# Kernel optimization log

Hardware: AMD Instinct MI355X
Metric: run time of the kernel (lower is better)

The kernel has to match this reference:

```python
import jax, jax.numpy as jnp
import numpy as np

B, T, C, H, W = 16, 8, 16, 64, 64
HID = 32          # round(sqrt(num_audio_input_ch * num_latent_ch)) = sqrt(16*64)
LAT = 64          # num_latent_ch
K = 3             # kernel_size


def conv(x, w, b):
    # x: [B,Cin,H,W], w: [Cout,Cin,K,K] (OIHW), SAME padding == padding (1,1) for 3x3
    y = jax.lax.conv_general_dilated(x, w, (1, 1), 'SAME',
                                     dimension_numbers=('NCHW', 'OIHW', 'NCHW'))
    return y + b[None, :, None, None]


def lstm_scan(x_seq, w, b, hid):
    # x_seq: [T,B,Cin,H,W] -> hidden sequence [T,B,hid,H,W]
    Bn, Hh, Ww = x_seq.shape[1], x_seq.shape[3], x_seq.shape[4]
    h0 = jnp.zeros((Bn, hid, Hh, Ww), x_seq.dtype)

    def step(carry, x_t):
        h, c = carry
        z = conv(jnp.concatenate([x_t, h], axis=1), w, b)     # [B,4*hid,H,W]
        i, f, o, g = jnp.split(z, 4, axis=1)                   # gate order i,f,o,g
        c2 = jax.nn.sigmoid(f) * c + jax.nn.sigmoid(i) * jnp.tanh(g)
        h2 = jax.nn.sigmoid(o) * jnp.tanh(c2)
        return (h2, c2), h2

    _, hs = jax.lax.scan(step, (h0, h0), x_seq)
    return hs


def bidir_layer(x_seq, wf, bf, wb, bb, hid):
    hf = lstm_scan(x_seq, wf, bf, hid)
    hb = jnp.flip(lstm_scan(jnp.flip(x_seq, 0), wb, bb, hid), 0)
    return jnp.concatenate([hf, hb], axis=2)                   # [T,B,2*hid,H,W]


def setup_inputs() -> dict:
    key = jax.random.key(0)
    ks = jax.random.split(key, 16)
    s = 0.05
    pe_dim = C * H * W
    inp = {
        'x_audio': jax.random.normal(ks[0], (B, T, C, H, W), jnp.float32),
        'midi_notes': jax.random.uniform(ks[1], (B, T, 2), jnp.float32, 0.0, 127.0),
        # note encoder: Linear(2,4) -> ReLU -> Linear(4, C*H*W) -> Tanh
        'enc_w1': jax.random.normal(ks[2], (2, 4), jnp.float32) * s,
        'enc_b1': jnp.zeros((4,), jnp.float32),
        'enc_w2': jax.random.normal(ks[3], (4, pe_dim), jnp.float32) * s,
        'enc_b2': jnp.zeros((pe_dim,), jnp.float32),
        # layer 0 (input C=16), fwd + bwd cells
        'w0f': jax.random.normal(ks[4], (4 * HID, C + HID, K, K), jnp.float32) * s,
        'b0f': jnp.zeros((4 * HID,), jnp.float32),
        'w0b': jax.random.normal(ks[5], (4 * HID, C + HID, K, K), jnp.float32) * s,
        'b0b': jnp.zeros((4 * HID,), jnp.float32),
        # layer 1 (input 2*HID=64)
        'w1f': jax.random.normal(ks[6], (4 * HID, 2 * HID + HID, K, K), jnp.float32) * s,
        'b1f': jnp.zeros((4 * HID,), jnp.float32),
        'w1b': jax.random.normal(ks[7], (4 * HID, 2 * HID + HID, K, K), jnp.float32) * s,
        'b1b': jnp.zeros((4 * HID,), jnp.float32),
        # final conv: 2*HID -> LAT
        'fc_w': jax.random.normal(ks[8], (LAT, 2 * HID, K, K), jnp.float32) * s,
        'fc_b': jnp.zeros((LAT,), jnp.float32),
    }
    return inp


def reference(x_audio, midi_notes, enc_w1, enc_b1, enc_w2, enc_b2,
              w0f, b0f, w0b, b0b, w1f, b1f, w1b, b1b, fc_w, fc_b):
    # positional encoding from MIDI notes, vectorized over all timesteps
    notes = -0.5 + midi_notes / 64.0                              # [B,T,2]
    pe = jnp.tanh(jax.nn.relu(notes @ enc_w1 + enc_b1) @ enc_w2 + enc_b2)  # [B,T,C*H*W]
    x = x_audio + pe.reshape(x_audio.shape)
    xs = jnp.transpose(x, (1, 0, 2, 3, 4))                        # [T,B,C,H,W]
    h = bidir_layer(xs, w0f, b0f, w0b, b0b, HID)                  # [T,B,64,H,W]
    h = bidir_layer(h, w1f, b1f, w1b, b1b, HID)                   # [T,B,64,H,W]
    return conv(h[-1], fc_w, fc_b)                                # [B,LAT,H,W]
```

## Files before the change

kernel.cpp:

```cpp
#include <hip/hip_runtime.h>

typedef _Float16 f16;
typedef _Float16 f16x8 __attribute__((ext_vector_type(8)));
typedef float f32x16 __attribute__((ext_vector_type(16)));

namespace {

constexpr int B_ = 16, T_ = 8, HW = 4096;

__device__ __forceinline__ float sigm(float x)  { return 1.f / (1.f + __expf(-x)); }
__device__ __forceinline__ float ftanh(float x) { return 1.f - 2.f / (1.f + __expf(2.f * x)); }

__device__ __forceinline__ f32x16 zero16() {
  f32x16 v;
#pragma unroll
  for (int i = 0; i < 16; ++i) v[i] = 0.f;
  return v;
}

__device__ __forceinline__ f16x8 zero8h() {
  f16x8 v;
#pragma unroll
  for (int i = 0; i < 8; ++i) v[i] = (f16)0.f;
  return v;
}

struct WSet { const float* src; f16* dst; int KC, NCO, CIN; };

__global__ void warr_kernel(WSet s0, WSet s1, WSet s2, WSet s3, WSet s4) {
  WSet s = s0;
  switch (blockIdx.y) { case 1: s = s1; break; case 2: s = s2; break;
                        case 3: s = s3; break; case 4: s = s4; break; default: break; }
  int n = 9 * s.KC * s.NCO * 16;
  int i = blockIdx.x * 256 + threadIdx.x;
  if (i >= n) return;
  int kk = i & 15;
  int t = i >> 4;
  int co = t % s.NCO;
  int dkc = t / s.NCO;
  int kc = dkc % s.KC, dydx = dkc / s.KC;
  int ci = kc * 16 + kk;
  float v = (ci < s.CIN) ? s.src[(co * s.CIN + ci) * 9 + dydx] : 0.f;
  s.dst[i] = (f16)v;
}

__global__ void pe_kernel(const float* __restrict__ xa, const float* __restrict__ midi,
                          const float* __restrict__ w1, const float* __restrict__ b1,
                          const float* __restrict__ w2, const float* __restrict__ b2,
                          f16* __restrict__ xs) {
  int gid = blockIdx.x * 256 + threadIdx.x;
  int half = gid & 1;
  int gpx = gid >> 1;
  int bt = gpx >> 12, gp = gpx & 4095;
  float n0 = -0.5f + midi[bt * 2 + 0] * (1.f / 64.f);
  float n1 = -0.5f + midi[bt * 2 + 1] * (1.f / 64.f);
  float hk[4];
#pragma unroll
  for (int k = 0; k < 4; ++k)
    hk[k] = fmaxf(fmaf(n0, w1[k], fmaf(n1, w1[4 + k], b1[k])), 0.f);
  f16x8 ov;
#pragma unroll
  for (int j = 0; j < 8; ++j) {
    int c = half * 8 + j;
    long p = (long)c * HW + gp;
    float z = b2[p];
#pragma unroll
    for (int k = 0; k < 4; ++k) z = fmaf(hk[k], w2[(long)k * 65536 + p], z);
    ov[j] = (f16)(xa[(long)bt * 65536 + p] + ftanh(z));
  }
  *reinterpret_cast<f16x8*>(xs + (long)gpx * 16 + half * 8) = ov;
}

struct ConvDir {
  const f16* x;  long xbs;
  const f16* h;  long hbs;
  const f16* w;
  const float* bias;
  const f16* cin;
  f16* cout;
  float* fout;
  f16* hout; long hobs;
};

template<int CIN1, int CIN2, int CINPAD, int KCF, int KC, int HST, int HOST,
         bool GATES, int NCO>
__global__ __launch_bounds__(256, 2)
void conv_mfma(ConvDir p0, ConvDir p1)
{
  constexpr int MFRAG = 2;
  constexpr int NF = NCO / 64;
  constexpr int NPH = 9 * KC;
  constexpr int ACT_BYTES = 180 * CINPAD * 2;
  constexpr int ZB_BYTES  = GATES ? 128 * 128 * 2 : 0;
  constexpr int SMEM = ACT_BYTES > ZB_BYTES ? ACT_BYTES : ZB_BYTES;
  __shared__ __align__(16) char smem[SMEM];
  f16* act = (f16*)smem;
  f16* zls = (f16*)smem;

  const ConvDir P = blockIdx.y ? p1 : p0;
  const int b = blockIdx.z;
  const int tileY = blockIdx.x >> 2, tileX = blockIdx.x & 3;
  const int gy0 = tileY * 8, gx0 = tileX * 16;
  const int tid = threadIdx.x;

  const int lane = tid & 63, wv = tid >> 6;
  const int mg = wv & 1, ng = wv >> 1;
  const int rl = lane & 31;
  const int khalf = (lane >> 5) * 8;
  const int laneA = ((rl >> 4) * 18 + (rl & 15)) * CINPAD + khalf;
  const int laneB = rl * 16 + khalf;
  const f16* __restrict__ wng = P.w + laneB + (long)ng * NF * 32 * 16;
  const f16* __restrict__ arow = act + laneA;

  constexpr int UPX = CIN1 / 8, UPH = CIN2 / 8, UPP = UPX + UPH;
  constexpr int NU  = 180 * UPP;
  constexpr int PER = (NU + 255) / 256;
  const bool have_h = (P.h != nullptr);
  f16x8 sreg[PER];
#pragma unroll
  for (int p = 0; p < PER; ++p) {
    sreg[p] = zero8h();
    int i = tid + p * 256;
    if (i < NU) {
      int px = i / UPP, u = i - px * UPP;
      int py = px / 18, pxx = px - py * 18;
      int gy = gy0 + py - 1, gx = gx0 + pxx - 1;
      if ((unsigned)gy < 64u && (unsigned)gx < 64u && (u < UPX || have_h)) {
        long gp = (long)gy * 64 + gx;
        const f16* src = (u < UPX) ? (P.x + b * P.xbs + gp * CIN1 + u * 8)
                                   : (P.h + b * P.hbs + gp * HST + (u - UPX) * 8);
        sreg[p] = *reinterpret_cast<const f16x8*>(src);
      }
    }
  }

  f16x8 bfr[3][NF];
  f16x8 afr[2][MFRAG];

  auto LBF = [&](int ph) {
    const int slot = ph % 3;
    const int dydx = ph / KC, kc = ph % KC;
#pragma unroll
    for (int nf = 0; nf < NF; ++nf)
      bfr[slot][nf] = *reinterpret_cast<const f16x8*>(
          wng + ((long)(dydx * KCF + kc) * NCO + nf * 32) * 16);
  };
  auto LAF = [&](int ph) {
    const int slot = ph & 1;
    const int dydx = ph / KC, kc = ph % KC;
    const int dy = dydx / 3, dx = dydx % 3;
#pragma unroll
    for (int m = 0; m < MFRAG; ++m)
      afr[slot][m] = *reinterpret_cast<const f16x8*>(
          arow + dx * CINPAD + (((mg * MFRAG + m) * 2 + dy) * 18) * CINPAD + kc * 16);
  };

  LBF(0);
  if (NPH > 1) LBF(1);

#pragma unroll
  for (int p = 0; p < PER; ++p) {
    int i = tid + p * 256;
    if (i < NU) {
      int px = i / UPP, u = i - px * UPP;
      *reinterpret_cast<f16x8*>(act + px * CINPAD + u * 8) = sreg[p];
    }
  }
  __syncthreads();

  if (NPH > 2) LBF(2);

  f32x16 acc[MFRAG][NF];
#pragma unroll
  for (int m = 0; m < MFRAG; ++m)
#pragma unroll
    for (int nf = 0; nf < NF; ++nf) acc[m][nf] = zero16();

  LAF(0);
#pragma unroll
  for (int ph = 0; ph < NPH; ++ph) {
    if (ph + 1 < NPH) LAF(ph + 1);
#pragma unroll
    for (int m = 0; m < MFRAG; ++m)
#pragma unroll
      for (int nf = 0; nf < NF; ++nf)
        acc[m][nf] = __builtin_amdgcn_mfma_f32_32x32x16_f16(
            afr[ph & 1][m], bfr[ph % 3][nf], acc[m][nf], 0, 0, 0);
    if (ph + 3 < NPH) LBF(ph + 3);
  }

  __syncthreads();

  if constexpr (GATES) {
#pragma unroll
    for (int m = 0; m < MFRAG; ++m) {
#pragma unroll
      for (int nf = 0; nf < NF; ++nf) {
        const int col = (ng * NF + nf) * 32 + rl;
        const float bs = P.bias[col];
#pragma unroll
        for (int r = 0; r < 16; ++r) {
          int row = (r & 3) + 8 * (r >> 2) + 4 * (lane >> 5);
          int px = (mg * MFRAG + m) * 32 + row;
          zls[px * 128 + col] = (f16)(acc[m][nf][r] + bs);
        }
      }
    }
    __syncthreads();
#pragma unroll
    for (int it = 0; it < 2; ++it) {
      const int idx = tid + it * 256;
      const int q = idx & 3, px = idx >> 2;
      const int py = px >> 4, pxx = px & 15;
      const long gp = (long)(gy0 + py) * 64 + (gx0 + pxx);
      const f16* zb = zls + px * 128 + q * 8;
      f16x8 zi8 = *reinterpret_cast<const f16x8*>(zb);
      f16x8 zf8 = *reinterpret_cast<const f16x8*>(zb + 32);
      f16x8 zo8 = *reinterpret_cast<const f16x8*>(zb + 64);
      f16x8 zg8 = *reinterpret_cast<const f16x8*>(zb + 96);
      const long cbase = ((long)b * HW + gp) * 32 + q * 8;
      f16x8 c8 = P.cin ? *reinterpret_cast<const f16x8*>(P.cin + cbase) : zero8h();
      f16x8 c2v, h2v;
#pragma unroll
      for (int j = 0; j < 8; ++j) {
        float c2 = sigm((float)zf8[j]) * (float)c8[j]
                 + sigm((float)zi8[j]) * ftanh((float)zg8[j]);
        c2v[j] = (f16)c2;
        h2v[j] = (f16)(sigm((float)zo8[j]) * ftanh(c2));
      }
      if (P.cout) *reinterpret_cast<f16x8*>(P.cout + cbase) = c2v;
      *reinterpret_cast<f16x8*>(P.hout + b * P.hobs + gp * HOST + q * 8) = h2v;
    }
  } else {
#pragma unroll
    for (int m = 0; m < MFRAG; ++m) {
#pragma unroll
      for (int nf = 0; nf < NF; ++nf) {
        const int co = (ng * NF + nf) * 32 + rl;
        const float bs = P.bias[co];
#pragma unroll
        for (int r = 0; r < 16; ++r) {
          int row = (r & 3) + 8 * (r >> 2) + 4 * (lane >> 5);
          int pxt = (mg * MFRAG + m) * 32 + row;
          int py = pxt >> 4, pxx = pxt & 15;
          long gp = (long)(gy0 + py) * 64 + (gx0 + pxx);
          P.fout[((long)b * NCO + co) * HW + gp] = acc[m][nf][r] + bs;
        }
      }
    }
  }
}

}

extern "C" void kernel_launch(void* const* d_in, const int* in_sizes, int n_in,
                              void* d_out, int out_size, void* d_ws, size_t ws_size,
                              hipStream_t stream) {
  const float* x_audio = (const float*)d_in[0];
  const float* midi    = (const float*)d_in[1];
  const float* enc_w1  = (const float*)d_in[2];
  const float* enc_b1  = (const float*)d_in[3];
  const float* enc_w2  = (const float*)d_in[4];
  const float* enc_b2  = (const float*)d_in[5];
  const float* w0f = (const float*)d_in[6];
  const float* b0f = (const float*)d_in[7];
  const float* w0b = (const float*)d_in[8];
  const float* b0b = (const float*)d_in[9];
  const float* w1f = (const float*)d_in[10];
  const float* b1f = (const float*)d_in[11];
  const float* w1b = (const float*)d_in[12];
  const float* b1b = (const float*)d_in[13];
  const float* fcw = (const float*)d_in[14];
  const float* fcb = (const float*)d_in[15];

  char* ws = (char*)d_ws;
  size_t off = 0;
  auto alloc = [&](size_t bytes) { char* p = ws + off; off += (bytes + 255) & ~(size_t)255; return p; };

  f16* xs    = (f16*)alloc((size_t)B_ * T_ * HW * 16 * 2);
  f16* seq0  = (f16*)alloc((size_t)T_ * B_ * HW * 64 * 2);
  f16* c0f   = (f16*)alloc((size_t)B_ * HW * 32 * 2);
  f16* c0b   = (f16*)alloc((size_t)B_ * HW * 32 * 2);
  f16* c1f   = (f16*)alloc((size_t)B_ * HW * 32 * 2);
  f16* h1p0  = (f16*)alloc((size_t)B_ * HW * 32 * 2);
  f16* h1p1  = (f16*)alloc((size_t)B_ * HW * 32 * 2);
  f16* h1bw  = (f16*)alloc((size_t)B_ * HW * 32 * 2);
  f16* wt0f  = (f16*)alloc((size_t)9 * 3 * 128 * 16 * 2);
  f16* wt0b  = (f16*)alloc((size_t)9 * 3 * 128 * 16 * 2);
  f16* wt1f  = (f16*)alloc((size_t)9 * 6 * 128 * 16 * 2);
  f16* wt1b  = (f16*)alloc((size_t)9 * 6 * 128 * 16 * 2);
  f16* wtfc  = (f16*)alloc((size_t)9 * 4 * 64 * 16 * 2);

  {
    WSet s0{w0f, wt0f, 3, 128, 48}, s1{w0b, wt0b, 3, 128, 48};
    WSet s2{w1f, wt1f, 6, 128, 96}, s3{w1b, wt1b, 6, 128, 96};
    WSet s4{fcw, wtfc, 4, 64, 64};
    warr_kernel<<<dim3(432, 5), 256, 0, stream>>>(s0, s1, s2, s3, s4);
  }

  pe_kernel<<<(B_ * T_ * HW * 2) / 256, 256, 0, stream>>>(
      x_audio, midi, enc_w1, enc_b1, enc_w2, enc_b2, xs);

  const long XSB  = (long)T_ * HW * 16;
  const long SLAB = (long)B_ * HW * 64;
  const long SB   = (long)HW * 64;
  const long HB   = (long)HW * 32;

  dim3 blk(256);

  {
    ConvDir f{xs, XSB, nullptr, SB, wt0f, b0f, nullptr, c0f, nullptr, seq0, SB};
    ConvDir r{xs + (long)7 * HW * 16, XSB, nullptr, SB, wt0b, b0b, nullptr, c0b,
              nullptr, seq0 + (long)7 * SLAB + 32, SB};
    conv_mfma<16, 32, 56, 3, 1, 64, 64, true, 128>
        <<<dim3(32, 2, 16), blk, 0, stream>>>(f, r);
  }
  for (int s = 1; s < 8; ++s) {
    int tf = s, tb = 7 - s;
    ConvDir f{xs + (long)tf * HW * 16, XSB,
              seq0 + (long)(tf - 1) * SLAB, SB,
              wt0f, b0f, c0f, (s == 7) ? nullptr : c0f, nullptr,
              seq0 + (long)tf * SLAB, SB};
    ConvDir r{xs + (long)tb * HW * 16, XSB,
              seq0 + (long)(tb + 1) * SLAB + 32, SB,
              wt0b, b0b, c0b, (s == 7) ? nullptr : c0b, nullptr,
              seq0 + (long)tb * SLAB + 32, SB};
    conv_mfma<16, 32, 56, 3, 3, 64, 64, true, 128>
        <<<dim3(32, 2, 16), blk, 0, stream>>>(f, r);
  }

  {
    ConvDir f{seq0, SB, nullptr, HB, wt1f, b1f, nullptr, c1f, nullptr, h1p0, HB};
    ConvDir r{seq0 + 7 * SLAB, SB, nullptr, HB, wt1b, b1b, nullptr, nullptr, nullptr, h1bw, HB};
    conv_mfma<64, 32, 104, 6, 4, 32, 32, true, 128>
        <<<dim3(32, 2, 16), blk, 0, stream>>>(f, r);
  }
  for (int s = 1; s < 8; ++s) {
    f16* hprev = (s & 1) ? h1p0 : h1p1;
    f16* hcur  = (s & 1) ? h1p1 : h1p0;
    ConvDir f{seq0 + (long)s * SLAB, SB, hprev, HB, wt1f, b1f,
              c1f, (s == 7) ? nullptr : c1f, nullptr, hcur, HB};
    conv_mfma<64, 32, 104, 6, 6, 32, 32, true, 128>
        <<<dim3(32, 1, 16), blk, 0, stream>>>(f, f);
  }

  {
    ConvDir f{h1p1, HB, h1bw, HB, wtfc, fcb, nullptr, nullptr, (float*)d_out, nullptr, 0};
    conv_mfma<32, 32, 72, 4, 4, 32, 32, false, 64>
        <<<dim3(32, 1, 16), blk, 0, stream>>>(f, f);
  }
}
```

Baseline: 462.8 us.

## Split conv K-loop across wave pairs with LDS reduction and halve tile height

Each block now covers a 4x16 pixel tile instead of 8x16, which doubles the grid. The 4 waves are split into 2 output-channel groups times 2 K-halves. Each K-half runs half the MFMA phases, and the partial accumulators are reduced through LDS before the gate epilogue. Launch bounds rise to 4 blocks per CU. The aim is more parallelism and occupancy for these small recurrent steps, at the cost of a larger halo fraction and extra LDS reduction traffic and syncs.

```diff
diff --git a/kernel.cpp b/kernel.cpp
--- a/kernel.cpp
+++ b/kernel.cpp
@@ -7,6 +7,8 @@
 namespace {
 
 constexpr int B_ = 16, T_ = 8, HW = 4096;
+
+template<int B2, int E2> struct Range { static constexpr int b = B2, e = E2; };
 
 __device__ __forceinline__ float sigm(float x)  { return 1.f / (1.f + __expf(-x)); }
 __device__ __forceinline__ float ftanh(float x) { return 1.f - 2.f / (1.f + __expf(2.f * x)); }
@@ -84,27 +86,32 @@
 
 template<int CIN1, int CIN2, int CINPAD, int KCF, int KC, int HST, int HOST,
          bool GATES, int NCO>
-__global__ __launch_bounds__(256, 2)
+__global__ __launch_bounds__(256, 4)
 void conv_mfma(ConvDir p0, ConvDir p1)
 {
-  constexpr int MFRAG = 2;
+  constexpr int MF = 2;
   constexpr int NF = NCO / 64;
   constexpr int NPH = 9 * KC;
-  constexpr int ACT_BYTES = 180 * CINPAD * 2;
-  constexpr int ZB_BYTES  = GATES ? 128 * 128 * 2 : 0;
-  constexpr int SMEM = ACT_BYTES > ZB_BYTES ? ACT_BYTES : ZB_BYTES;
-  __shared__ __align__(16) char smem[SMEM];
-  f16* act = (f16*)smem;
-  f16* zls = (f16*)smem;
+  constexpr int PH0 = (NPH + 1) / 2;
+  constexpr int NFRAGS = MF * NF;
+  constexpr int ACT_BYTES = 108 * CINPAD * 2;
+  constexpr int RED_BYTES = 2 * NFRAGS * 64 * 16 * 4;
+  constexpr int ZB_BYTES  = GATES ? 64 * 128 * 2 : 0;
+  constexpr int SM1 = ACT_BYTES > RED_BYTES ? ACT_BYTES : RED_BYTES;
+  constexpr int SMEM = SM1 > ZB_BYTES ? SM1 : ZB_BYTES;
+  __shared__ __align__(64) char smem[SMEM];
+  f16*   act = (f16*)smem;
+  float* red = (float*)smem;
+  f16*   zls = (f16*)smem;
 
   const ConvDir P = blockIdx.y ? p1 : p0;
   const int b = blockIdx.z;
   const int tileY = blockIdx.x >> 2, tileX = blockIdx.x & 3;
-  const int gy0 = tileY * 8, gx0 = tileX * 16;
+  const int gy0 = tileY * 4, gx0 = tileX * 16;
   const int tid = threadIdx.x;
 
   const int lane = tid & 63, wv = tid >> 6;
-  const int mg = wv & 1, ng = wv >> 1;
+  const int ng = wv & 1, ks = wv >> 1;
   const int rl = lane & 31;
   const int khalf = (lane >> 5) * 8;
   const int laneA = ((rl >> 4) * 18 + (rl & 15)) * CINPAD + khalf;
@@ -113,7 +120,7 @@
   const f16* __restrict__ arow = act + laneA;
 
   constexpr int UPX = CIN1 / 8, UPH = CIN2 / 8, UPP = UPX + UPH;
-  constexpr int NU  = 180 * UPP;
+  constexpr int NU  = 108 * UPP;
   constexpr int PER = (NU + 255) / 256;
   const bool have_h = (P.h != nullptr);
   f16x8 sreg[PER];
@@ -133,9 +140,22 @@
       }
     }
   }
+#pragma unroll
+  for (int p = 0; p < PER; ++p) {
+    int i = tid + p * 256;
+    if (i < NU) {
+      int px = i / UPP, u = i - px * UPP;
+      *reinterpret_cast<f16x8*>(act + px * CINPAD + u * 8) = sreg[p];
+    }
+  }
 
   f16x8 bfr[3][NF];
-  f16x8 afr[2][MFRAG];
+  f16x8 afr[2][MF];
+  f32x16 acc[MF][NF];
+#pragma unroll
+  for (int m = 0; m < MF; ++m)
+#pragma unroll
+    for (int nf = 0; nf < NF; ++nf) acc[m][nf] = zero16();
 
   auto LBF = [&](int ph) {
     const int slot = ph % 3;
@@ -150,101 +170,108 @@
     const int dydx = ph / KC, kc = ph % KC;
     const int dy = dydx / 3, dx = dydx % 3;
 #pragma unroll
-    for (int m = 0; m < MFRAG; ++m)
+    for (int m = 0; m < MF; ++m)
       afr[slot][m] = *reinterpret_cast<const f16x8*>(
-          arow + dx * CINPAD + (((mg * MFRAG + m) * 2 + dy) * 18) * CINPAD + kc * 16);
+          arow + dx * CINPAD + ((m * 2 + dy) * 18) * CINPAD + kc * 16);
   };
 
-  LBF(0);
-  if (NPH > 1) LBF(1);
-
-#pragma unroll
-  for (int p = 0; p < PER; ++p) {
-    int i = tid + p * 256;
-    if (i < NU) {
-      int px = i / UPP, u = i - px * UPP;
-      *reinterpret_cast<f16x8*>(act + px * CINPAD + u * 8) = sreg[p];
-    }
-  }
   __syncthreads();
 
-  if (NPH > 2) LBF(2);
-
-  f32x16 acc[MFRAG][NF];
-#pragma unroll
-  for (int m = 0; m < MFRAG; ++m)
-#pragma unroll
-    for (int nf = 0; nf < NF; ++nf) acc[m][nf] = zero16();
-
-  LAF(0);
-#pragma unroll
-  for (int ph = 0; ph < NPH; ++ph) {
-    if (ph + 1 < NPH) LAF(ph + 1);
-#pragma unroll
-    for (int m = 0; m < MFRAG; ++m)
+  auto KLOOP = [&](auto rng) {
+    constexpr int BEG = decltype(rng)::b;
+    constexpr int END = decltype(rng)::e;
+    LBF(BEG);
+    if constexpr (BEG + 1 < END) LBF(BEG + 1);
+    if constexpr (BEG + 2 < END) LBF(BEG + 2);
+    LAF(BEG);
+#pragma unroll
+    for (int ph = BEG; ph < END; ++ph) {
+      if (ph + 1 < END) LAF(ph + 1);
+#pragma unroll
+      for (int m = 0; m < MF; ++m)
+#pragma unroll
+        for (int nf = 0; nf < NF; ++nf)
+          acc[m][nf] = __builtin_amdgcn_mfma_f32_32x32x16_f16(
+              afr[ph & 1][m], bfr[ph % 3][nf], acc[m][nf], 0, 0, 0);
+      if (ph + 3 < END) LBF(ph + 3);
+    }
+  };
+  if (ks == 0) KLOOP(Range<0, PH0>{});
+  else         KLOOP(Range<PH0, NPH>{});
+
+  __syncthreads();
+  if (ks == 1) {
+#pragma unroll
+    for (int m = 0; m < MF; ++m)
 #pragma unroll
       for (int nf = 0; nf < NF; ++nf)
-        acc[m][nf] = __builtin_amdgcn_mfma_f32_32x32x16_f16(
-            afr[ph & 1][m], bfr[ph % 3][nf], acc[m][nf], 0, 0, 0);
-    if (ph + 3 < NPH) LBF(ph + 3);
-  }
-
+        *reinterpret_cast<f32x16*>(
+            red + (((ng * NFRAGS + m * NF + nf) * 64) + lane) * 16) = acc[m][nf];
+  }
   __syncthreads();
+  if (ks == 0) {
+#pragma unroll
+    for (int m = 0; m < MF; ++m)
+#pragma unroll
+      for (int nf = 0; nf < NF; ++nf)
+        acc[m][nf] += *reinterpret_cast<const f32x16*>(
+            red + (((ng * NFRAGS + m * NF + nf) * 64) + lane) * 16);
+  }
 
   if constexpr (GATES) {
-#pragma unroll
-    for (int m = 0; m < MFRAG; ++m) {
-#pragma unroll
-      for (int nf = 0; nf < NF; ++nf) {
-        const int col = (ng * NF + nf) * 32 + rl;
-        const float bs = P.bias[col];
-#pragma unroll
-        for (int r = 0; r < 16; ++r) {
-          int row = (r & 3) + 8 * (r >> 2) + 4 * (lane >> 5);
-          int px = (mg * MFRAG + m) * 32 + row;
-          zls[px * 128 + col] = (f16)(acc[m][nf][r] + bs);
+    __syncthreads();
+    if (ks == 0) {
+#pragma unroll
+      for (int m = 0; m < MF; ++m) {
+#pragma unroll
+        for (int nf = 0; nf < NF; ++nf) {
+          const int col = (ng * NF + nf) * 32 + rl;
+          const float bs = P.bias[col];
+#pragma unroll
+          for (int r = 0; r < 16; ++r) {
+            int row = (r & 3) + 8 * (r >> 2) + 4 * (lane >> 5);
+            zls[(m * 32 + row) * 128 + col] = (f16)(acc[m][nf][r] + bs);
+          }
         }
       }
     }
     __syncthreads();
-#pragma unroll
-    for (int it = 0; it < 2; ++it) {
-      const int idx = tid + it * 256;
-      const int q = idx & 3, px = idx >> 2;
-      const int py = px >> 4, pxx = px & 15;
-      const long gp = (long)(gy0 + py) * 64 + (gx0 + pxx);
-      const f16* zb = zls + px * 128 + q * 8;
-      f16x8 zi8 = *reinterpret_cast<const f16x8*>(zb);
-      f16x8 zf8 = *reinterpret_cast<const f16x8*>(zb + 32);
-      f16x8 zo8 = *reinterpret_cast<const f16x8*>(zb + 64);
-      f16x8 zg8 = *reinterpret_cast<const f16x8*>(zb + 96);
-      const long cbase = ((long)b * HW + gp) * 32 + q * 8;
-      f16x8 c8 = P.cin ? *reinterpret_cast<const f16x8*>(P.cin + cbase) : zero8h();
-      f16x8 c2v, h2v;
-#pragma unroll
-      for (int j = 0; j < 8; ++j) {
-        float c2 = sigm((float)zf8[j]) * (float)c8[j]
-                 + sigm((float)zi8[j]) * ftanh((float)zg8[j]);
-        c2v[j] = (f16)c2;
-        h2v[j] = (f16)(sigm((float)zo8[j]) * ftanh(c2));
-      }
-      if (P.cout) *reinterpret_cast<f16x8*>(P.cout + cbase) = c2v;
-      *reinterpret_cast<f16x8*>(P.hout + b * P.hobs + gp * HOST + q * 8) = h2v;
-    }
+    const int q = tid & 3, px = tid >> 2;
+    const int py = px >> 4, pxx = px & 15;
+    const long gp = (long)(gy0 + py) * 64 + (gx0 + pxx);
+    const f16* zb = zls + px * 128 + q * 8;
+    f16x8 zi8 = *reinterpret_cast<const f16x8*>(zb);
+    f16x8 zf8 = *reinterpret_cast<const f16x8*>(zb + 32);
+    f16x8 zo8 = *reinterpret_cast<const f16x8*>(zb + 64);
+    f16x8 zg8 = *reinterpret_cast<const f16x8*>(zb + 96);
+    const long cbase = ((long)b * HW + gp) * 32 + q * 8;
+    f16x8 c8 = P.cin ? *reinterpret_cast<const f16x8*>(P.cin + cbase) : zero8h();
+    f16x8 c2v, h2v;
+#pragma unroll
+    for (int j = 0; j < 8; ++j) {
+      float c2 = sigm((float)zf8[j]) * (float)c8[j]
+               + sigm((float)zi8[j]) * ftanh((float)zg8[j]);
+      c2v[j] = (f16)c2;
+      h2v[j] = (f16)(sigm((float)zo8[j]) * ftanh(c2));
+    }
+    if (P.cout) *reinterpret_cast<f16x8*>(P.cout + cbase) = c2v;
+    *reinterpret_cast<f16x8*>(P.hout + b * P.hobs + gp * HOST + q * 8) = h2v;
   } else {
-#pragma unroll
-    for (int m = 0; m < MFRAG; ++m) {
-#pragma unroll
-      for (int nf = 0; nf < NF; ++nf) {
-        const int co = (ng * NF + nf) * 32 + rl;
-        const float bs = P.bias[co];
-#pragma unroll
-        for (int r = 0; r < 16; ++r) {
-          int row = (r & 3) + 8 * (r >> 2) + 4 * (lane >> 5);
-          int pxt = (mg * MFRAG + m) * 32 + row;
-          int py = pxt >> 4, pxx = pxt & 15;
-          long gp = (long)(gy0 + py) * 64 + (gx0 + pxx);
-          P.fout[((long)b * NCO + co) * HW + gp] = acc[m][nf][r] + bs;
+    if (ks == 0) {
+#pragma unroll
+      for (int m = 0; m < MF; ++m) {
+#pragma unroll
+        for (int nf = 0; nf < NF; ++nf) {
+          const int co = (ng * NF + nf) * 32 + rl;
+          const float bs = P.bias[co];
+#pragma unroll
+          for (int r = 0; r < 16; ++r) {
+            int row = (r & 3) + 8 * (r >> 2) + 4 * (lane >> 5);
+            int pxt = m * 32 + row;
+            int py = pxt >> 4, pxx = pxt & 15;
+            long gp = (long)(gy0 + py) * 64 + (gx0 + pxx);
+            P.fout[((long)b * NCO + co) * HW + gp] = acc[m][nf][r] + bs;
+          }
         }
       }
     }
@@ -313,7 +340,7 @@
     ConvDir r{xs + (long)7 * HW * 16, XSB, nullptr, SB, wt0b, b0b, nullptr, c0b,
               nullptr, seq0 + (long)7 * SLAB + 32, SB};
     conv_mfma<16, 32, 56, 3, 1, 64, 64, true, 128>
-        <<<dim3(32, 2, 16), blk, 0, stream>>>(f, r);
+        <<<dim3(64, 2, 16), blk, 0, stream>>>(f, r);
   }
   for (int s = 1; s < 8; ++s) {
     int tf = s, tb = 7 - s;
@@ -326,14 +353,14 @@
               wt0b, b0b, c0b, (s == 7) ? nullptr : c0b, nullptr,
               seq0 + (long)tb * SLAB + 32, SB};
     conv_mfma<16, 32, 56, 3, 3, 64, 64, true, 128>
-        <<<dim3(32, 2, 16), blk, 0, stream>>>(f, r);
+        <<<dim3(64, 2, 16), blk, 0, stream>>>(f, r);
   }
 
   {
     ConvDir f{seq0, SB, nullptr, HB, wt1f, b1f, nullptr, c1f, nullptr, h1p0, HB};
     ConvDir r{seq0 + 7 * SLAB, SB, nullptr, HB, wt1b, b1b, nullptr, nullptr, nullptr, h1bw, HB};
     conv_mfma<64, 32, 104, 6, 4, 32, 32, true, 128>
-        <<<dim3(32, 2, 16), blk, 0, stream>>>(f, r);
+        <<<dim3(64, 2, 16), blk, 0, stream>>>(f, r);
   }
   for (int s = 1; s < 8; ++s) {
     f16* hprev = (s & 1) ? h1p0 : h1p1;
@@ -341,12 +368,12 @@
     ConvDir f{seq0 + (long)s * SLAB, SB, hprev, HB, wt1f, b1f,
               c1f, (s == 7) ? nullptr : c1f, nullptr, hcur, HB};
     conv_mfma<64, 32, 104, 6, 6, 32, 32, true, 128>
-        <<<dim3(32, 1, 16), blk, 0, stream>>>(f, f);
+        <<<dim3(64, 1, 16), blk, 0, stream>>>(f, f);
   }
 
   {
     ConvDir f{h1p1, HB, h1bw, HB, wtfc, fcb, nullptr, nullptr, (float*)d_out, nullptr, 0};
     conv_mfma<32, 32, 72, 4, 4, 32, 32, false, 64>
-        <<<dim3(32, 1, 16), blk, 0, stream>>>(f, f);
-  }
-}
+        <<<dim3(64, 1, 16), blk, 0, stream>>>(f, f);
+  }
+}
```

After: 517.5 us. 1.12x slower.

## Hoist layer-1 input convolution out of the recurrent loop into one batched kernel

Applied to the files above, without the earlier changes.

Splits the layer-1 forward LSTM conv into an input part (64 channels from seq0) and a recurrent part (32 channels from h). A new kernel computes the input part for all 7 later timesteps, plus the first forward and the backward step, in one wide launch and stores the pre-activations in a new f16 buffer. Each sequential step then only convolves the 32-channel hidden state and adds the stored input part before the gates. This removes input-conv work from the serial dependency chain, at the cost of an extra global write and read of the 128-channel pre-activations and one more round of f16 rounding on them.

```diff
diff --git a/kernel.cpp b/kernel.cpp
--- a/kernel.cpp
+++ b/kernel.cpp
@@ -25,12 +25,13 @@
   return v;
 }
 
-struct WSet { const float* src; f16* dst; int KC, NCO, CIN; };
-
-__global__ void warr_kernel(WSet s0, WSet s1, WSet s2, WSet s3, WSet s4) {
+struct WSet { const float* src; f16* dst; int KC, NCO, CIN, coff; };
+
+__global__ void warr_kernel(WSet s0, WSet s1, WSet s2, WSet s3, WSet s4, WSet s5) {
   WSet s = s0;
   switch (blockIdx.y) { case 1: s = s1; break; case 2: s = s2; break;
-                        case 3: s = s3; break; case 4: s = s4; break; default: break; }
+                        case 3: s = s3; break; case 4: s = s4; break;
+                        case 5: s = s5; break; default: break; }
   int n = 9 * s.KC * s.NCO * 16;
   int i = blockIdx.x * 256 + threadIdx.x;
   if (i >= n) return;
@@ -39,7 +40,7 @@
   int co = t % s.NCO;
   int dkc = t / s.NCO;
   int kc = dkc % s.KC, dydx = dkc / s.KC;
-  int ci = kc * 16 + kk;
+  int ci = s.coff + kc * 16 + kk;
   float v = (ci < s.CIN) ? s.src[(co * s.CIN + ci) * 9 + dydx] : 0.f;
   s.dst[i] = (f16)v;
 }
@@ -80,6 +81,7 @@
   f16* cout;
   float* fout;
   f16* hout; long hobs;
+  const f16* zx;
 };
 
 template<int CIN1, int CIN2, int CINPAD, int KCF, int KC, int HST, int HOST,
@@ -197,7 +199,7 @@
 #pragma unroll
       for (int nf = 0; nf < NF; ++nf) {
         const int col = (ng * NF + nf) * 32 + rl;
-        const float bs = P.bias[col];
+        const float bs = P.bias ? P.bias[col] : 0.f;
 #pragma unroll
         for (int r = 0; r < 16; ++r) {
           int row = (r & 3) + 8 * (r >> 2) + 4 * (lane >> 5);
@@ -218,15 +220,26 @@
       f16x8 zf8 = *reinterpret_cast<const f16x8*>(zb + 32);
       f16x8 zo8 = *reinterpret_cast<const f16x8*>(zb + 64);
       f16x8 zg8 = *reinterpret_cast<const f16x8*>(zb + 96);
+      f16x8 xi8 = zero8h(), xf8 = zero8h(), xo8 = zero8h(), xg8 = zero8h();
+      if (P.zx) {
+        const f16* zxb = P.zx + ((long)b * HW + gp) * 128 + q * 8;
+        xi8 = *reinterpret_cast<const f16x8*>(zxb);
+        xf8 = *reinterpret_cast<const f16x8*>(zxb + 32);
+        xo8 = *reinterpret_cast<const f16x8*>(zxb + 64);
+        xg8 = *reinterpret_cast<const f16x8*>(zxb + 96);
+      }
       const long cbase = ((long)b * HW + gp) * 32 + q * 8;
       f16x8 c8 = P.cin ? *reinterpret_cast<const f16x8*>(P.cin + cbase) : zero8h();
       f16x8 c2v, h2v;
 #pragma unroll
       for (int j = 0; j < 8; ++j) {
-        float c2 = sigm((float)zf8[j]) * (float)c8[j]
-                 + sigm((float)zi8[j]) * ftanh((float)zg8[j]);
+        float zi = (float)zi8[j] + (float)xi8[j];
+        float zf = (float)zf8[j] + (float)xf8[j];
+        float zo = (float)zo8[j] + (float)xo8[j];
+        float zg = (float)zg8[j] + (float)xg8[j];
+        float c2 = sigm(zf) * (float)c8[j] + sigm(zi) * ftanh(zg);
         c2v[j] = (f16)c2;
-        h2v[j] = (f16)(sigm((float)zo8[j]) * ftanh(c2));
+        h2v[j] = (f16)(sigm(zo) * ftanh(c2));
       }
       if (P.cout) *reinterpret_cast<f16x8*>(P.cout + cbase) = c2v;
       *reinterpret_cast<f16x8*>(P.hout + b * P.hobs + gp * HOST + q * 8) = h2v;
@@ -246,6 +259,162 @@
           long gp = (long)(gy0 + py) * 64 + (gx0 + pxx);
           P.fout[((long)b * NCO + co) * HW + gp] = acc[m][nf][r] + bs;
         }
+      }
+    }
+  }
+}
+
+__global__ __launch_bounds__(256, 2)
+void zx_kernel(const f16* __restrict__ seq0,
+               const f16* __restrict__ wxf, const f16* __restrict__ wxb,
+               const float* __restrict__ bf, const float* __restrict__ bb,
+               f16* __restrict__ zx, f16* __restrict__ h1p0,
+               f16* __restrict__ c1f, f16* __restrict__ h1bw)
+{
+  constexpr int CINPAD = 72, KC = 4, NPH = 36, NF = 2, MFRAG = 2;
+  constexpr int ACT_BYTES = 180 * CINPAD * 2;
+  constexpr int SMEM = 128 * 128 * 2;
+  __shared__ __align__(16) char smem[SMEM];
+  f16* act = (f16*)smem;
+  f16* zls = (f16*)smem;
+
+  const int sd = blockIdx.x >> 5;
+  const int t32 = blockIdx.x & 31;
+  const int b = blockIdx.z;
+  const int tileY = t32 >> 2, tileX = t32 & 3;
+  const int gy0 = tileY * 8, gx0 = tileX * 16;
+  const int tid = threadIdx.x;
+
+  const int t = (sd == 8) ? 7 : sd;
+  const f16* __restrict__ x = seq0 + (long)t * B_ * HW * 64;
+  const f16* __restrict__ w = (sd == 8) ? wxb : wxf;
+  const float* __restrict__ bias = (sd == 8) ? bb : bf;
+
+  const int lane = tid & 63, wv = tid >> 6;
+  const int mg = wv & 1, ng = wv >> 1;
+  const int rl = lane & 31;
+  const int khalf = (lane >> 5) * 8;
+  const int laneA = ((rl >> 4) * 18 + (rl & 15)) * CINPAD + khalf;
+  const int laneB = rl * 16 + khalf;
+  const f16* __restrict__ wng = w + laneB + (long)ng * NF * 32 * 16;
+  const f16* __restrict__ arow = act + laneA;
+
+  constexpr int UPP = 8, NU = 180 * UPP, PER = (NU + 255) / 256;
+  f16x8 sreg[PER];
+#pragma unroll
+  for (int p = 0; p < PER; ++p) {
+    sreg[p] = zero8h();
+    int i = tid + p * 256;
+    if (i < NU) {
+      int px = i / UPP, u = i - px * UPP;
+      int py = px / 18, pxx = px - py * 18;
+      int gy = gy0 + py - 1, gx = gx0 + pxx - 1;
+      if ((unsigned)gy < 64u && (unsigned)gx < 64u) {
+        long gp = (long)gy * 64 + gx;
+        sreg[p] = *reinterpret_cast<const f16x8*>(
+            x + ((long)b * HW + gp) * 64 + u * 8);
+      }
+    }
+  }
+
+  f16x8 bfr[3][NF];
+  f16x8 afr[2][MFRAG];
+  auto LBF = [&](int ph) {
+    const int slot = ph % 3;
+    const int dydx = ph / KC, kc = ph % KC;
+#pragma unroll
+    for (int nf = 0; nf < NF; ++nf)
+      bfr[slot][nf] = *reinterpret_cast<const f16x8*>(
+          wng + ((long)(dydx * KC + kc) * 128 + nf * 32) * 16);
+  };
+  auto LAF = [&](int ph) {
+    const int slot = ph & 1;
+    const int dydx = ph / KC, kc = ph % KC;
+    const int dy = dydx / 3, dx = dydx % 3;
+#pragma unroll
+    for (int m = 0; m < MFRAG; ++m)
+      afr[slot][m] = *reinterpret_cast<const f16x8*>(
+          arow + dx * CINPAD + (((mg * MFRAG + m) * 2 + dy) * 18) * CINPAD + kc * 16);
+  };
+
+  LBF(0); LBF(1);
+#pragma unroll
+  for (int p = 0; p < PER; ++p) {
+    int i = tid + p * 256;
+    if (i < NU) {
+      int px = i / UPP, u = i - px * UPP;
+      *reinterpret_cast<f16x8*>(act + px * CINPAD + u * 8) = sreg[p];
+    }
+  }
+  __syncthreads();
+  LBF(2);
+
+  f32x16 acc[MFRAG][NF];
+#pragma unroll
+  for (int m = 0; m < MFRAG; ++m)
+#pragma unroll
+    for (int nf = 0; nf < NF; ++nf) acc[m][nf] = zero16();
+
+  LAF(0);
+#pragma unroll
+  for (int ph = 0; ph < NPH; ++ph) {
+    if (ph + 1 < NPH) LAF(ph + 1);
+#pragma unroll
+    for (int m = 0; m < MFRAG; ++m)
+#pragma unroll
+      for (int nf = 0; nf < NF; ++nf)
+        acc[m][nf] = __builtin_amdgcn_mfma_f32_32x32x16_f16(
+            afr[ph & 1][m], bfr[ph % 3][nf], acc[m][nf], 0, 0, 0);
+    if (ph + 3 < NPH) LBF(ph + 3);
+  }
+
+  __syncthreads();
+#pragma unroll
+  for (int m = 0; m < MFRAG; ++m) {
+#pragma unroll
+    for (int nf = 0; nf < NF; ++nf) {
+      const int col = (ng * NF + nf) * 32 + rl;
+      const float bs = bias[col];
+#pragma unroll
+      for (int r = 0; r < 16; ++r) {
+        int row = (r & 3) + 8 * (r >> 2) + 4 * (lane >> 5);
+        int px = (mg * MFRAG + m) * 32 + row;
+        zls[px * 128 + col] = (f16)(acc[m][nf][r] + bs);
+      }
+    }
+  }
+  __syncthreads();
+#pragma unroll
+  for (int it = 0; it < 2; ++it) {
+    const int idx = tid + it * 256;
+    const int q = idx & 3, px = idx >> 2;
+    const int py = px >> 4, pxx = px & 15;
+    const long gp = (long)(gy0 + py) * 64 + (gx0 + pxx);
+    const f16* zb = zls + px * 128 + q * 8;
+    f16x8 zi8 = *reinterpret_cast<const f16x8*>(zb);
+    f16x8 zf8 = *reinterpret_cast<const f16x8*>(zb + 32);
+    f16x8 zo8 = *reinterpret_cast<const f16x8*>(zb + 64);
+    f16x8 zg8 = *reinterpret_cast<const f16x8*>(zb + 96);
+    if (sd >= 1 && sd <= 7) {
+      f16* dst = zx + (((long)(sd - 1) * B_ + b) * HW + gp) * 128 + q * 8;
+      *reinterpret_cast<f16x8*>(dst)      = zi8;
+      *reinterpret_cast<f16x8*>(dst + 32) = zf8;
+      *reinterpret_cast<f16x8*>(dst + 64) = zo8;
+      *reinterpret_cast<f16x8*>(dst + 96) = zg8;
+    } else {
+      f16x8 c2v, h2v;
+#pragma unroll
+      for (int j = 0; j < 8; ++j) {
+        float c2 = sigm((float)zi8[j]) * ftanh((float)zg8[j]);
+        c2v[j] = (f16)c2;
+        h2v[j] = (f16)(sigm((float)zo8[j]) * ftanh(c2));
+      }
+      const long hb = ((long)b * HW + gp) * 32 + q * 8;
+      if (sd == 0) {
+        *reinterpret_cast<f16x8*>(h1p0 + hb) = h2v;
+        *reinterpret_cast<f16x8*>(c1f + hb)  = c2v;
+      } else {
+        *reinterpret_cast<f16x8*>(h1bw + hb) = h2v;
       }
     }
   }
@@ -279,6 +448,7 @@
 
   f16* xs    = (f16*)alloc((size_t)B_ * T_ * HW * 16 * 2);
   f16* seq0  = (f16*)alloc((size_t)T_ * B_ * HW * 64 * 2);
+  f16* zx1   = (f16*)alloc((size_t)7 * B_ * HW * 128 * 2);
   f16* c0f   = (f16*)alloc((size_t)B_ * HW * 32 * 2);
   f16* c0b   = (f16*)alloc((size_t)B_ * HW * 32 * 2);
   f16* c1f   = (f16*)alloc((size_t)B_ * HW * 32 * 2);
@@ -287,15 +457,17 @@
   f16* h1bw  = (f16*)alloc((size_t)B_ * HW * 32 * 2);
   f16* wt0f  = (f16*)alloc((size_t)9 * 3 * 128 * 16 * 2);
   f16* wt0b  = (f16*)alloc((size_t)9 * 3 * 128 * 16 * 2);
-  f16* wt1f  = (f16*)alloc((size_t)9 * 6 * 128 * 16 * 2);
-  f16* wt1b  = (f16*)alloc((size_t)9 * 6 * 128 * 16 * 2);
+  f16* wx1f  = (f16*)alloc((size_t)9 * 4 * 128 * 16 * 2);
+  f16* wx1b  = (f16*)alloc((size_t)9 * 4 * 128 * 16 * 2);
+  f16* wh1f  = (f16*)alloc((size_t)9 * 2 * 128 * 16 * 2);
   f16* wtfc  = (f16*)alloc((size_t)9 * 4 * 64 * 16 * 2);
 
   {
-    WSet s0{w0f, wt0f, 3, 128, 48}, s1{w0b, wt0b, 3, 128, 48};
-    WSet s2{w1f, wt1f, 6, 128, 96}, s3{w1b, wt1b, 6, 128, 96};
-    WSet s4{fcw, wtfc, 4, 64, 64};
-    warr_kernel<<<dim3(432, 5), 256, 0, stream>>>(s0, s1, s2, s3, s4);
+    WSet s0{w0f, wt0f, 3, 128, 48, 0}, s1{w0b, wt0b, 3, 128, 48, 0};
+    WSet s2{w1f, wx1f, 4, 128, 96, 0}, s3{w1b, wx1b, 4, 128, 96, 0};
+    WSet s4{w1f, wh1f, 2, 128, 96, 64};
+    WSet s5{fcw, wtfc, 4, 64, 64, 0};
+    warr_kernel<<<dim3(288, 6), 256, 0, stream>>>(s0, s1, s2, s3, s4, s5);
   }
 
   pe_kernel<<<(B_ * T_ * HW * 2) / 256, 256, 0, stream>>>(
@@ -309,9 +481,9 @@
   dim3 blk(256);
 
   {
-    ConvDir f{xs, XSB, nullptr, SB, wt0f, b0f, nullptr, c0f, nullptr, seq0, SB};
+    ConvDir f{xs, XSB, nullptr, SB, wt0f, b0f, nullptr, c0f, nullptr, seq0, SB, nullptr};
     ConvDir r{xs + (long)7 * HW * 16, XSB, nullptr, SB, wt0b, b0b, nullptr, c0b,
-              nullptr, seq0 + (long)7 * SLAB + 32, SB};
+              nullptr, seq0 + (long)7 * SLAB + 32, SB, nullptr};
     conv_mfma<16, 32, 56, 3, 1, 64, 64, true, 128>
         <<<dim3(32, 2, 16), blk, 0, stream>>>(f, r);
   }
@@ -320,32 +492,31 @@
     ConvDir f{xs + (long)tf * HW * 16, XSB,
               seq0 + (long)(tf - 1) * SLAB, SB,
               wt0f, b0f, c0f, (s == 7) ? nullptr : c0f, nullptr,
-              seq0 + (long)tf * SLAB, SB};
+              seq0 + (long)tf * SLAB, SB, nullptr};
     ConvDir r{xs + (long)tb * HW * 16, XSB,
               seq0 + (long)(tb + 1) * SLAB + 32, SB,
               wt0b, b0b, c0b, (s == 7) ? nullptr : c0b, nullptr,
-              seq0 + (long)tb * SLAB + 32, SB};
+              seq0 + (long)tb * SLAB + 32, SB, nullptr};
     conv_mfma<16, 32, 56, 3, 3, 64, 64, true, 128>
         <<<dim3(32, 2, 16), blk, 0, stream>>>(f, r);
   }
 
-  {
-    ConvDir f{seq0, SB, nullptr, HB, wt1f, b1f, nullptr, c1f, nullptr, h1p0, HB};
-    ConvDir r{seq0 + 7 * SLAB, SB, nullptr, HB, wt1b, b1b, nullptr, nullptr, nullptr, h1bw, HB};
-    conv_mfma<64, 32, 104, 6, 4, 32, 32, true, 128>
-        <<<dim3(32, 2, 16), blk, 0, stream>>>(f, r);
-  }
+  zx_kernel<<<dim3(32 * 9, 1, 16), blk, 0, stream>>>(
+      seq0, wx1f, wx1b, b1f, b1b, zx1, h1p0, c1f, h1bw);
+
   for (int s = 1; s < 8; ++s) {
     f16* hprev = (s & 1) ? h1p0 : h1p1;
     f16* hcur  = (s & 1) ? h1p1 : h1p0;
-    ConvDir f{seq0 + (long)s * SLAB, SB, hprev, HB, wt1f, b1f,
-              c1f, (s == 7) ? nullptr : c1f, nullptr, hcur, HB};
-    conv_mfma<64, 32, 104, 6, 6, 32, 32, true, 128>
+    ConvDir f{hprev, HB, nullptr, 0, wh1f, nullptr,
+              c1f, (s == 7) ? nullptr : c1f, nullptr, hcur, HB,
+              zx1 + (long)(s - 1) * B_ * HW * 128};
+    conv_mfma<32, 0, 40, 2, 2, 32, 32, true, 128>
         <<<dim3(32, 1, 16), blk, 0, stream>>>(f, f);
   }
 
   {
-    ConvDir f{h1p1, HB, h1bw, HB, wtfc, fcb, nullptr, nullptr, (float*)d_out, nullptr, 0};
+    ConvDir f{h1p1, HB, h1bw, HB, wtfc, fcb, nullptr, nullptr, (float*)d_out,
+              nullptr, 0, nullptr};
     conv_mfma<32, 32, 72, 4, 4, 32, 32, false, 64>
         <<<dim3(32, 1, 16), blk, 0, stream>>>(f, f);
   }
```

Measured after the change: 497.5 us. +7.5%, slower.
